# Kernel optimization log

Hardware: AMD Instinct MI355X
Metric: run time of the kernel (lower is better)

## Reference

```python
import jax, jax.numpy as jnp
import numpy as np

N = 8192
D_IN = 512
D_HID = 256
D_OUT = 128
NEG_SLOPE = 0.25
MASK_VAL = -1.0e12
EDGE_PROB = 0.004  # avg degree ~33


def _leaky(x):
    return jax.nn.leaky_relu(x, NEG_SLOPE)


def setup_inputs() -> dict:
    key = jax.random.key(0)
    ks = jax.random.split(key, 9)
    x = jax.random.normal(ks[0], (N, D_IN), jnp.float32)
    # sparse-ish normalized adjacency, stored dense (torch uses sparse mm / to_dense)
    vals = jax.random.uniform(ks[1], (N, N), jnp.float32)
    mask = jax.random.uniform(ks[2], (N, N)) < EDGE_PROB
    adj = jnp.where(mask, vals, 0.0).astype(jnp.float32)
    W1 = jax.random.normal(ks[3], (D_IN, D_HID), jnp.float32) * (2.0 / (D_IN + D_HID)) ** 0.5
    b1 = jnp.zeros((D_HID,), jnp.float32)
    W2 = jax.random.normal(ks[4], (D_HID, D_HID), jnp.float32) * (1.0 / D_HID) ** 0.5
    b2 = jnp.zeros((D_HID,), jnp.float32)
    Wg = jax.random.normal(ks[5], (D_HID, D_OUT), jnp.float32) * (2.0 / (D_HID + D_OUT)) ** 0.5
    a = jax.random.normal(ks[6], (2 * D_OUT, 1), jnp.float32) * 0.1
    return dict(x=x, adj=adj, W1=W1, b1=b1, W2=W2, b2=b2, Wg=Wg, a=a)


def reference(x, adj, W1, b1, W2, b2, Wg, a):
    # GCN layer 1: adj @ (x @ W1) + b1, leaky_relu (dropout p=0 / eval -> identity)
    x1 = _leaky(adj @ (x @ W1) + b1)
    # GCN layer 2
    x2 = _leaky(adj @ (x1 @ W2) + b2)
    # GAT layer: h = x2 @ Wg; e[i,j] = leaky_relu([h_i || h_j] @ a)
    # identical to leaky_relu((h@a1)_i + (h@a2)_j) without the O(N^2*2F) concat
    h = x2 @ Wg                              # [N, D_OUT]
    a1 = a[:D_OUT, 0]
    a2 = a[D_OUT:, 0]
    e = _leaky((h @ a1)[:, None] + (h @ a2)[None, :])  # [N, N]
    att = jnp.where(adj > 0, e, MASK_VAL)
    att = jax.nn.softmax(att, axis=1)
    h_prime = att @ h                        # [N, D_OUT] (concat=False -> no elu)
    out = _leaky(h_prime)
    mu = out[:, : D_OUT // 2]
    logvar = out[:, D_OUT // 2 :]
    return mu, logvar
```

## Files before the change

kernel.cpp:

```cpp
#include <hip/hip_runtime.h>

typedef unsigned short u16;
typedef u16 u16x4 __attribute__((ext_vector_type(4)));
typedef __bf16 bf16x8 __attribute__((ext_vector_type(8)));
typedef float f32x4 __attribute__((ext_vector_type(4)));

#define NROW 8192
#define CAP 128
#define D_IN 512
#define D_HID 256
#define D_OUT 128

__device__ __forceinline__ float leaky_f(float x) { return x > 0.f ? x : 0.25f * x; }

__device__ __forceinline__ u16 f2bf_rne(float f) {
  unsigned u = __float_as_uint(f);
  u += 0x7fffu + ((u >> 16) & 1u);
  return (u16)(u >> 16);
}
__device__ __forceinline__ void split_bf16(float f, u16& hi, u16& lo) {
  hi = f2bf_rne(f);
  float fh = __uint_as_float(((unsigned)hi) << 16);
  lo = f2bf_rne(f - fh);
}

__global__ __launch_bounds__(256) void k_csr(const float* __restrict__ adj,
    int* __restrict__ cnt, int* __restrict__ cols, float* __restrict__ vals) {
  int i = blockIdx.x;
  __shared__ int c;
  if (threadIdx.x == 0) c = 0;
  __syncthreads();
  const float4* row = (const float4*)(adj + (size_t)i * NROW);
  for (int j4 = threadIdx.x; j4 < NROW / 4; j4 += 256) {
    float4 v = row[j4];
    int base = j4 * 4;
    if (v.x > 0.f) { int s = atomicAdd(&c, 1); if (s < CAP) { cols[i*CAP+s] = base;   vals[i*CAP+s] = v.x; } }
    if (v.y > 0.f) { int s = atomicAdd(&c, 1); if (s < CAP) { cols[i*CAP+s] = base+1; vals[i*CAP+s] = v.y; } }
    if (v.z > 0.f) { int s = atomicAdd(&c, 1); if (s < CAP) { cols[i*CAP+s] = base+2; vals[i*CAP+s] = v.z; } }
    if (v.w > 0.f) { int s = atomicAdd(&c, 1); if (s < CAP) { cols[i*CAP+s] = base+3; vals[i*CAP+s] = v.w; } }
  }
  __syncthreads();
  if (threadIdx.x == 0) cnt[i] = (c < CAP) ? c : CAP;
}

__global__ __launch_bounds__(256) void k_pack_all(const float* __restrict__ X, u16* __restrict__ Ap,
    const float* __restrict__ W1, u16* __restrict__ B1,
    const float* __restrict__ W2, u16* __restrict__ B2,
    const float* __restrict__ Wg, u16* __restrict__ B3) {
  int b = blockIdx.x;
  if (b < 16384) {
    size_t id = (size_t)b * 256 + threadIdx.x;
    int k = (int)(id & 511);
    size_t i = id >> 9;
    float f = X[id];
    u16 hi, lo; split_bf16(f, hi, lo);
    size_t ro = i * 1024;
    Ap[ro + k] = hi; Ap[ro + 512 + k] = lo;
    return;
  }
  const float* W; u16* Bt; int K, Nc, id;
  if (b < 16896)      { W = W1; Bt = B1; K = D_IN;  Nc = D_HID; id = (b - 16384) * 256 + threadIdx.x; }
  else if (b < 17152) { W = W2; Bt = B2; K = D_HID; Nc = D_HID; id = (b - 16896) * 256 + threadIdx.x; }
  else                { W = Wg; Bt = B3; K = D_HID; Nc = D_OUT; id = (b - 17152) * 256 + threadIdx.x; }
  if (id >= K * Nc) return;
  int n = id % Nc, k = id / Nc;
  float f = W[id];
  u16 hi, lo; split_bf16(f, hi, lo);
  size_t ro = (size_t)n * 2 * K;
  Bt[ro + k] = hi; Bt[ro + K + k] = lo;
}

__global__ __launch_bounds__(256) void k_gemm(const u16* __restrict__ A, const u16* __restrict__ Bt,
    float* __restrict__ C, int N, int K,
    const float* __restrict__ aptr, float* __restrict__ s1, float* __restrict__ s2) {
  __shared__ u16 Ah[64 * 40], Al[64 * 40];
  __shared__ u16 Bh[128 * 40], Bl[128 * 40];
  int tid = threadIdx.x;
  int bm = blockIdx.y * 64, bn = blockIdx.x * 128;
  int wave = tid >> 6, lane = tid & 63, l15 = lane & 15, quad = lane >> 4;
  f32x4 acc[8] = {};
  int ar = tid >> 2, aj = (tid & 3) << 3;
  int br = tid >> 1, bj0 = (tid & 1) << 4;
  const u16* Arow = A + (size_t)(bm + ar) * (2 * K);
  const u16* Brow = Bt + (size_t)(bn + br) * (2 * K);
  for (int k0 = 0; k0 < K; k0 += 32) {
    *(uint4*)(&Ah[ar * 40 + aj]) = *(const uint4*)(Arow + k0 + aj);
    *(uint4*)(&Al[ar * 40 + aj]) = *(const uint4*)(Arow + K + k0 + aj);
#pragma unroll
    for (int jj = 0; jj < 2; ++jj) {
      *(uint4*)(&Bh[br * 40 + bj0 + jj * 8]) = *(const uint4*)(Brow + k0 + bj0 + jj * 8);
      *(uint4*)(&Bl[br * 40 + bj0 + jj * 8]) = *(const uint4*)(Brow + K + k0 + bj0 + jj * 8);
    }
    __syncthreads();
    bf16x8 afh = *(const bf16x8*)(&Ah[(wave * 16 + l15) * 40 + quad * 8]);
    bf16x8 afl = *(const bf16x8*)(&Al[(wave * 16 + l15) * 40 + quad * 8]);
#pragma unroll
    for (int c = 0; c < 8; ++c) {
      bf16x8 bfh = *(const bf16x8*)(&Bh[(c * 16 + l15) * 40 + quad * 8]);
      bf16x8 bfl = *(const bf16x8*)(&Bl[(c * 16 + l15) * 40 + quad * 8]);
      acc[c] = __builtin_amdgcn_mfma_f32_16x16x32_bf16(afh, bfh, acc[c], 0, 0, 0);
      acc[c] = __builtin_amdgcn_mfma_f32_16x16x32_bf16(afh, bfl, acc[c], 0, 0, 0);
      acc[c] = __builtin_amdgcn_mfma_f32_16x16x32_bf16(afl, bfh, acc[c], 0, 0, 0);
    }
    __syncthreads();
  }
#pragma unroll
  for (int c = 0; c < 8; ++c)
#pragma unroll
    for (int rg = 0; rg < 4; ++rg) {
      int rowi = bm + wave * 16 + quad * 4 + rg;
      int coli = bn + c * 16 + l15;
      C[(size_t)rowi * N + coli] = acc[c][rg];
    }
  if (aptr) {
    float a1v[8], a2v[8];
#pragma unroll
    for (int c = 0; c < 8; ++c) { a1v[c] = aptr[c * 16 + l15]; a2v[c] = aptr[128 + c * 16 + l15]; }
#pragma unroll
    for (int rg = 0; rg < 4; ++rg) {
      float p1 = 0.f, p2 = 0.f;
#pragma unroll
      for (int c = 0; c < 8; ++c) { p1 = fmaf(acc[c][rg], a1v[c], p1); p2 = fmaf(acc[c][rg], a2v[c], p2); }
#pragma unroll
      for (int m = 1; m < 16; m <<= 1) { p1 += __shfl_xor(p1, m); p2 += __shfl_xor(p2, m); }
      if (l15 == 0) {
        int rowi = bm + wave * 16 + quad * 4 + rg;
        s1[rowi] = p1; s2[rowi] = p2;
      }
    }
  }
}

__global__ __launch_bounds__(256) void k_spmm_pack(const float* __restrict__ Hin,
    const float* __restrict__ bias, const int* __restrict__ cnt,
    const int* __restrict__ cols, const float* __restrict__ vals, u16* __restrict__ Ap) {
  int i = blockIdx.x, t = threadIdx.x;
  int t64 = t & 63, g = t >> 6;
  __shared__ int sc[CAP];
  __shared__ float sv[CAP];
  __shared__ float4 sacc[4][64];
  int n = cnt[i];
  if (t < n) { sc[t] = cols[i * CAP + t]; sv[t] = vals[i * CAP + t]; }
  __syncthreads();
  float4 acc = {0.f, 0.f, 0.f, 0.f};
  const float4* H4 = (const float4*)Hin;
  for (int k = g; k < n; k += 4) {
    float w = sv[k];
    float4 v = H4[(size_t)sc[k] * 64 + t64];
    acc.x = fmaf(w, v.x, acc.x); acc.y = fmaf(w, v.y, acc.y);
    acc.z = fmaf(w, v.z, acc.z); acc.w = fmaf(w, v.w, acc.w);
  }
  sacc[g][t64] = acc;
  __syncthreads();
  if (t < 64) {
    float4 a0 = sacc[0][t], a1 = sacc[1][t], a2 = sacc[2][t], a3 = sacc[3][t];
    float4 bv = ((const float4*)bias)[t];
    float r[4] = { leaky_f(a0.x + a1.x + a2.x + a3.x + bv.x),
                   leaky_f(a0.y + a1.y + a2.y + a3.y + bv.y),
                   leaky_f(a0.z + a1.z + a2.z + a3.z + bv.z),
                   leaky_f(a0.w + a1.w + a2.w + a3.w + bv.w) };
    u16x4 hi4, lo4;
#pragma unroll
    for (int e = 0; e < 4; ++e) { u16 hh, ll; split_bf16(r[e], hh, ll); hi4[e] = hh; lo4[e] = ll; }
    size_t ro = (size_t)i * 512;
    *(u16x4*)(Ap + ro + 4 * t) = hi4;
    *(u16x4*)(Ap + ro + 256 + 4 * t) = lo4;
  }
}

__global__ __launch_bounds__(128) void k_attn(const float* __restrict__ h,
    const float* __restrict__ s1, const float* __restrict__ s2,
    const int* __restrict__ cnt, const int* __restrict__ cols, float* __restrict__ out) {
  int i = blockIdx.x, t = threadIdx.x;
  int t32 = t & 31, g = t >> 5;
  __shared__ int sc[CAP];
  __shared__ float sw[CAP];
  __shared__ float sred[2];
  __shared__ float4 sacc[4][32];
  int n = cnt[i];
  float s1i = s1[i];
  if (t < n) { int c = cols[i * CAP + t]; sc[t] = c; sw[t] = leaky_f(s1i + s2[c]); }
  __syncthreads();
  if (t < 64) {
    float m = -1e30f;
    if (t < n) m = sw[t];
    if (t + 64 < n) m = fmaxf(m, sw[t + 64]);
    for (int o = 32; o > 0; o >>= 1) m = fmaxf(m, __shfl_down(m, o));
    if (t == 0) sred[0] = m;
  }
  __syncthreads();
  float mx = sred[0];
  if (t < n) sw[t] = expf(sw[t] - mx);
  __syncthreads();
  if (t < 64) {
    float s = 0.f;
    if (t < n) s = sw[t];
    if (t + 64 < n) s += sw[t + 64];
    for (int o = 32; o > 0; o >>= 1) s += __shfl_down(s, o);
    if (t == 0) sred[1] = s;
  }
  __syncthreads();
  float inv = (n > 0) ? 1.0f / sred[1] : 0.f;
  float4 acc = {0.f, 0.f, 0.f, 0.f};
  const float4* h4 = (const float4*)h;
  for (int k = g; k < n; k += 4) {
    float w = sw[k];
    float4 v = h4[(size_t)sc[k] * 32 + t32];
    acc.x = fmaf(w, v.x, acc.x); acc.y = fmaf(w, v.y, acc.y);
    acc.z = fmaf(w, v.z, acc.z); acc.w = fmaf(w, v.w, acc.w);
  }
  sacc[g][t32] = acc;
  __syncthreads();
  if (t < 32) {
    float4 a0 = sacc[0][t], a1 = sacc[1][t], a2 = sacc[2][t], a3 = sacc[3][t];
    float4 r;
    r.x = leaky_f((a0.x + a1.x + a2.x + a3.x) * inv);
    r.y = leaky_f((a0.y + a1.y + a2.y + a3.y) * inv);
    r.z = leaky_f((a0.z + a1.z + a2.z + a3.z) * inv);
    r.w = leaky_f((a0.w + a1.w + a2.w + a3.w) * inv);
    float4* o4 = (float4*)out;
    if (t < 16) o4[(size_t)i * 16 + t] = r;
    else        o4[(size_t)NROW * 16 + (size_t)i * 16 + (t - 16)] = r;
  }
}

extern "C" void kernel_launch(void* const* d_in, const int* in_sizes, int n_in,
                              void* d_out, int out_size, void* d_ws, size_t ws_size,
                              hipStream_t stream) {
  const float* x   = (const float*)d_in[0];
  const float* adj = (const float*)d_in[1];
  const float* W1  = (const float*)d_in[2];
  const float* b1  = (const float*)d_in[3];
  const float* W2  = (const float*)d_in[4];
  const float* b2  = (const float*)d_in[5];
  const float* Wg  = (const float*)d_in[6];
  const float* a   = (const float*)d_in[7];
  float* out = (float*)d_out;

  char* ws = (char*)d_ws;
  int*   row_cnt  = (int*)  (ws + 0);
  int*   row_cols = (int*)  (ws + 32768);
  float* row_vals = (float*)(ws + 4227072);
  u16*   B1t      = (u16*)  (ws + 8421376);
  u16*   B2t      = (u16*)  (ws + 8945664);
  u16*   B3t      = (u16*)  (ws + 9207808);
  float* s1       = (float*)(ws + 9338880);
  float* s2       = (float*)(ws + 9371648);
  float* h        = (float*)(ws + 9404416);
  float* H0T2     = (float*)(ws + 13598720);
  u16*   Apack    = (u16*)  (ws + 21987328);

  k_csr<<<NROW, 256, 0, stream>>>(adj, row_cnt, row_cols, row_vals);
  k_pack_all<<<17280, 256, 0, stream>>>(x, Apack, W1, B1t, W2, B2t, Wg, B3t);
  k_gemm<<<dim3(2, 128), 256, 0, stream>>>(Apack, B1t, H0T2, D_HID, D_IN, nullptr, nullptr, nullptr);
  k_spmm_pack<<<NROW, 256, 0, stream>>>(H0T2, b1, row_cnt, row_cols, row_vals, Apack);
  k_gemm<<<dim3(2, 128), 256, 0, stream>>>(Apack, B2t, H0T2, D_HID, D_HID, nullptr, nullptr, nullptr);
  k_spmm_pack<<<NROW, 256, 0, stream>>>(H0T2, b2, row_cnt, row_cols, row_vals, Apack);
  k_gemm<<<dim3(1, 128), 256, 0, stream>>>(Apack, B3t, h, D_OUT, D_HID, a, s1, s2);
  k_attn<<<NROW, 128, 0, stream>>>(h, s1, s2, row_cnt, row_cols, out);
}
```

Baseline: 502.2 us.

## Fuse x bf16 split into first GEMM and merge CSR build with weight packing

The standalone pass that split x into packed hi/lo bf16 is removed. The first GEMM now loads fp32 x directly and splits it while staging into shared memory, which avoids writing and rereading a 16 MB packed buffer. The CSR build and the weight-packing blocks are merged into one launch to save a kernel launch. In exchange, the GEMM does the split arithmetic inside its load path, and x tiles that are shared across the two column blocks are converted twice.

```diff
diff --git a/kernel.cpp b/kernel.cpp
--- a/kernel.cpp
+++ b/kernel.cpp
@@ -24,50 +24,89 @@
   lo = f2bf_rne(f - fh);
 }
 
-__global__ __launch_bounds__(256) void k_csr(const float* __restrict__ adj,
-    int* __restrict__ cnt, int* __restrict__ cols, float* __restrict__ vals) {
-  int i = blockIdx.x;
-  __shared__ int c;
-  if (threadIdx.x == 0) c = 0;
-  __syncthreads();
-  const float4* row = (const float4*)(adj + (size_t)i * NROW);
-  for (int j4 = threadIdx.x; j4 < NROW / 4; j4 += 256) {
-    float4 v = row[j4];
-    int base = j4 * 4;
-    if (v.x > 0.f) { int s = atomicAdd(&c, 1); if (s < CAP) { cols[i*CAP+s] = base;   vals[i*CAP+s] = v.x; } }
-    if (v.y > 0.f) { int s = atomicAdd(&c, 1); if (s < CAP) { cols[i*CAP+s] = base+1; vals[i*CAP+s] = v.y; } }
-    if (v.z > 0.f) { int s = atomicAdd(&c, 1); if (s < CAP) { cols[i*CAP+s] = base+2; vals[i*CAP+s] = v.z; } }
-    if (v.w > 0.f) { int s = atomicAdd(&c, 1); if (s < CAP) { cols[i*CAP+s] = base+3; vals[i*CAP+s] = v.w; } }
-  }
-  __syncthreads();
-  if (threadIdx.x == 0) cnt[i] = (c < CAP) ? c : CAP;
-}
-
-__global__ __launch_bounds__(256) void k_pack_all(const float* __restrict__ X, u16* __restrict__ Ap,
+__global__ __launch_bounds__(256) void k_csr_packw(const float* __restrict__ adj,
+    int* __restrict__ cnt, int* __restrict__ cols, float* __restrict__ vals,
     const float* __restrict__ W1, u16* __restrict__ B1,
     const float* __restrict__ W2, u16* __restrict__ B2,
     const float* __restrict__ Wg, u16* __restrict__ B3) {
   int b = blockIdx.x;
-  if (b < 16384) {
-    size_t id = (size_t)b * 256 + threadIdx.x;
-    int k = (int)(id & 511);
-    size_t i = id >> 9;
-    float f = X[id];
-    u16 hi, lo; split_bf16(f, hi, lo);
-    size_t ro = i * 1024;
-    Ap[ro + k] = hi; Ap[ro + 512 + k] = lo;
+  if (b < NROW) {
+    int i = b;
+    __shared__ int c;
+    if (threadIdx.x == 0) c = 0;
+    __syncthreads();
+    const float4* row = (const float4*)(adj + (size_t)i * NROW);
+    for (int j4 = threadIdx.x; j4 < NROW / 4; j4 += 256) {
+      float4 v = row[j4];
+      int base = j4 * 4;
+      if (v.x > 0.f) { int s = atomicAdd(&c, 1); if (s < CAP) { cols[i*CAP+s] = base;   vals[i*CAP+s] = v.x; } }
+      if (v.y > 0.f) { int s = atomicAdd(&c, 1); if (s < CAP) { cols[i*CAP+s] = base+1; vals[i*CAP+s] = v.y; } }
+      if (v.z > 0.f) { int s = atomicAdd(&c, 1); if (s < CAP) { cols[i*CAP+s] = base+2; vals[i*CAP+s] = v.z; } }
+      if (v.w > 0.f) { int s = atomicAdd(&c, 1); if (s < CAP) { cols[i*CAP+s] = base+3; vals[i*CAP+s] = v.w; } }
+    }
+    __syncthreads();
+    if (threadIdx.x == 0) cnt[i] = (c < CAP) ? c : CAP;
     return;
   }
   const float* W; u16* Bt; int K, Nc, id;
-  if (b < 16896)      { W = W1; Bt = B1; K = D_IN;  Nc = D_HID; id = (b - 16384) * 256 + threadIdx.x; }
-  else if (b < 17152) { W = W2; Bt = B2; K = D_HID; Nc = D_HID; id = (b - 16896) * 256 + threadIdx.x; }
-  else                { W = Wg; Bt = B3; K = D_HID; Nc = D_OUT; id = (b - 17152) * 256 + threadIdx.x; }
-  if (id >= K * Nc) return;
+  int pb = b - NROW;
+  if (pb < 512)      { W = W1; Bt = B1; K = D_IN;  Nc = D_HID; id = pb * 256 + threadIdx.x; }
+  else if (pb < 768) { W = W2; Bt = B2; K = D_HID; Nc = D_HID; id = (pb - 512) * 256 + threadIdx.x; }
+  else               { W = Wg; Bt = B3; K = D_HID; Nc = D_OUT; id = (pb - 768) * 256 + threadIdx.x; }
   int n = id % Nc, k = id / Nc;
   float f = W[id];
   u16 hi, lo; split_bf16(f, hi, lo);
   size_t ro = (size_t)n * 2 * K;
   Bt[ro + k] = hi; Bt[ro + K + k] = lo;
+}
+
+__global__ __launch_bounds__(256) void k_gemm_x(const float* __restrict__ X, const u16* __restrict__ Bt,
+    float* __restrict__ C, int N, int K) {
+  __shared__ u16 Ah[64 * 40], Al[64 * 40];
+  __shared__ u16 Bh[128 * 40], Bl[128 * 40];
+  int tid = threadIdx.x;
+  int bm = blockIdx.y * 64, bn = blockIdx.x * 128;
+  int wave = tid >> 6, lane = tid & 63, l15 = lane & 15, quad = lane >> 4;
+  f32x4 acc[8] = {};
+  int ar = tid >> 2, aj = (tid & 3) << 3;
+  int br = tid >> 1, bj0 = (tid & 1) << 4;
+  const float* Xrow = X + (size_t)(bm + ar) * K + aj;
+  const u16* Brow = Bt + (size_t)(bn + br) * (2 * K);
+  for (int k0 = 0; k0 < K; k0 += 32) {
+    alignas(16) u16 hh[8], ll[8];
+    float xv[8];
+    *(float4*)(xv)     = *(const float4*)(Xrow + k0);
+    *(float4*)(xv + 4) = *(const float4*)(Xrow + k0 + 4);
+#pragma unroll
+    for (int e = 0; e < 8; ++e) split_bf16(xv[e], hh[e], ll[e]);
+    *(uint4*)(&Ah[ar * 40 + aj]) = *(const uint4*)hh;
+    *(uint4*)(&Al[ar * 40 + aj]) = *(const uint4*)ll;
+#pragma unroll
+    for (int jj = 0; jj < 2; ++jj) {
+      *(uint4*)(&Bh[br * 40 + bj0 + jj * 8]) = *(const uint4*)(Brow + k0 + bj0 + jj * 8);
+      *(uint4*)(&Bl[br * 40 + bj0 + jj * 8]) = *(const uint4*)(Brow + K + k0 + bj0 + jj * 8);
+    }
+    __syncthreads();
+    bf16x8 afh = *(const bf16x8*)(&Ah[(wave * 16 + l15) * 40 + quad * 8]);
+    bf16x8 afl = *(const bf16x8*)(&Al[(wave * 16 + l15) * 40 + quad * 8]);
+#pragma unroll
+    for (int c = 0; c < 8; ++c) {
+      bf16x8 bfh = *(const bf16x8*)(&Bh[(c * 16 + l15) * 40 + quad * 8]);
+      bf16x8 bfl = *(const bf16x8*)(&Bl[(c * 16 + l15) * 40 + quad * 8]);
+      acc[c] = __builtin_amdgcn_mfma_f32_16x16x32_bf16(afh, bfh, acc[c], 0, 0, 0);
+      acc[c] = __builtin_amdgcn_mfma_f32_16x16x32_bf16(afh, bfl, acc[c], 0, 0, 0);
+      acc[c] = __builtin_amdgcn_mfma_f32_16x16x32_bf16(afl, bfh, acc[c], 0, 0, 0);
+    }
+    __syncthreads();
+  }
+#pragma unroll
+  for (int c = 0; c < 8; ++c)
+#pragma unroll
+    for (int rg = 0; rg < 4; ++rg) {
+      int rowi = bm + wave * 16 + quad * 4 + rg;
+      int coli = bn + c * 16 + l15;
+      C[(size_t)rowi * N + coli] = acc[c][rg];
+    }
 }
 
 __global__ __launch_bounds__(256) void k_gemm(const u16* __restrict__ A, const u16* __restrict__ Bt,
@@ -250,9 +289,9 @@
   float* H0T2     = (float*)(ws + 13598720);
   u16*   Apack    = (u16*)  (ws + 21987328);
 
-  k_csr<<<NROW, 256, 0, stream>>>(adj, row_cnt, row_cols, row_vals);
-  k_pack_all<<<17280, 256, 0, stream>>>(x, Apack, W1, B1t, W2, B2t, Wg, B3t);
-  k_gemm<<<dim3(2, 128), 256, 0, stream>>>(Apack, B1t, H0T2, D_HID, D_IN, nullptr, nullptr, nullptr);
+  k_csr_packw<<<NROW + 896, 256, 0, stream>>>(adj, row_cnt, row_cols, row_vals,
+                                              W1, B1t, W2, B2t, Wg, B3t);
+  k_gemm_x<<<dim3(2, 128), 256, 0, stream>>>(x, B1t, H0T2, D_HID, D_IN);
   k_spmm_pack<<<NROW, 256, 0, stream>>>(H0T2, b1, row_cnt, row_cols, row_vals, Apack);
   k_gemm<<<dim3(2, 128), 256, 0, stream>>>(Apack, B2t, H0T2, D_HID, D_HID, nullptr, nullptr, nullptr);
   k_spmm_pack<<<NROW, 256, 0, stream>>>(H0T2, b2, row_cnt, row_cols, row_vals, Apack);
```

New measurement: 494.8 us. Within noise of the previous version (-1.5%).
